# Kernel optimization log

Measured on AMD Instinct MI355X. Metric: run time of the kernel, lower is better.

The kernel has to match this reference:

```python
import jax, jax.numpy as jnp
import numpy as np

D_MODEL = 1024
H = 16
D_K = D_MODEL // H
EPS = 1e-8


def _feature_map(x):
    # elu(x) + 1 (Performer/linear-attention positive feature map)
    return jax.nn.elu(x) + 1.0


def setup_inputs() -> dict:
    key = jax.random.key(0)
    ks = jax.random.split(key, 8)
    B, L = 4, 2048
    q = jax.random.normal(ks[0], (B, L, D_MODEL), dtype=jnp.float32)
    k = jax.random.normal(ks[1], (B, L, D_MODEL), dtype=jnp.float32)
    v = jax.random.normal(ks[2], (B, L, D_MODEL), dtype=jnp.float32)
    mask = jnp.ones((B, 1, 1, L), dtype=bool)
    s = 1.0 / np.sqrt(D_MODEL)
    w_q = jax.random.normal(ks[3], (D_MODEL, D_MODEL), dtype=jnp.float32) * s
    w_k = jax.random.normal(ks[4], (D_MODEL, D_MODEL), dtype=jnp.float32) * s
    w_v = jax.random.normal(ks[5], (D_MODEL, D_MODEL), dtype=jnp.float32) * s
    w_o = jax.random.normal(ks[6], (D_MODEL, D_MODEL), dtype=jnp.float32) * s
    return {"q": q, "k": k, "v": v, "mask": mask,
            "w_q": w_q, "w_k": w_k, "w_v": w_v, "w_o": w_o}


def reference(q, k, v, mask, w_q, w_k, w_v, w_o):
    # Linear (use_Linear=True) branch of MultiHeadAttentionBlock.forward.
    B, Lq, _ = q.shape
    Lk = k.shape[1]
    # fused-style projections (torch Linear: x @ W.T), split into heads -> bhnd
    query = (q @ w_q.T).reshape(B, Lq, H, D_K).transpose(0, 2, 1, 3)
    key_  = (k @ w_k.T).reshape(B, Lk, H, D_K).transpose(0, 2, 1, 3)
    value = (v @ w_v.T).reshape(B, Lk, H, D_K).transpose(0, 2, 1, 3)

    Q = _feature_map(query)            # [B,H,Lq,d_k]
    K = _feature_map(key_)             # [B,H,Lk,d_k]
    KV = jnp.einsum('bhnd,bhnm->bhdm', K, value)           # [B,H,d_k,d_k]
    Z = 1.0 / (jnp.einsum('bhnd,bhd->bhn', Q, K.sum(axis=2)) + EPS)  # [B,H,Lq]
    out = jnp.einsum('bhnd,bhdm,bhn->bhnm', Q, KV, Z)      # [B,H,Lq,d_k]

    out = out.transpose(0, 2, 1, 3).reshape(B, Lq, D_MODEL)
    return out @ w_o.T
```

## Files before the change

### kernel.cpp

```cpp
#include <hip/hip_runtime.h>
#include <cstdint>
#include <cstddef>

typedef __bf16 bf16;
typedef __bf16 bf16x8 __attribute__((ext_vector_type(8)));
typedef __bf16 bf16x4 __attribute__((ext_vector_type(4)));
typedef float  f32x4  __attribute__((ext_vector_type(4)));

#define DM     1024
#define MROWS  8192
#define LSEQ   2048
#define NBATCH 4
#define NHEAD  16
#define BHEADS 64
#define KV_S   8
#define KVT_STRIDE 4160

__device__ __forceinline__ void async16(const void* g, void* l) {
    __builtin_amdgcn_global_load_lds(
        (const __attribute__((address_space(1))) void*)g,
        (__attribute__((address_space(3))) void*)l, 16, 0, 0);
}

struct CastArgs {
    const float* s[7];
    bf16*        d[7];
    int          nblk[7];
};

__global__ __launch_bounds__(256) void cast_all(CastArgs a) {
    const int z = blockIdx.z;
    if ((int)blockIdx.x >= a.nblk[z]) return;
    const int i = blockIdx.x * 256 + threadIdx.x;
    float4 f = ((const float4*)a.s[z])[i];
    bf16x4 o; o[0] = (bf16)f.x; o[1] = (bf16)f.y; o[2] = (bf16)f.z; o[3] = (bf16)f.w;
    ((bf16x4*)a.d[z])[i] = o;
}

struct GemmArgs {
    const bf16* A[3];
    const bf16* B[3];
    void*       C[3];
    int         mode[3];
    int         Ndim;
    int         Kdim;
};

__global__ __launch_bounds__(256) void gemm_nt(GemmArgs args) {
    const int z = blockIdx.z;
    const bf16* __restrict__ A  = args.A[z];
    const bf16* __restrict__ Bm = args.B[z];
    void* Cp = args.C[z];
    const int mode = args.mode[z];
    const int N = args.Ndim, K = args.Kdim;

    __shared__ __attribute__((aligned(16))) bf16 sA[128 * 64];
    __shared__ __attribute__((aligned(16))) bf16 sB[128 * 64];

    const int tid  = threadIdx.x;
    const int wave = tid >> 6;
    const int lane = tid & 63;
    const int wm = wave >> 1, wn = wave & 1;

    const int fb = blockIdx.x + 8 * (int)blockIdx.y;
    const int bx = (fb >> 3) & 7;
    const int by = (fb & 7) * 8 + (fb >> 6);
    const int row0 = by * 128;
    const int col0 = bx * 128;

    const int rr = lane >> 3;
    const int cc = lane & 7;
    const int csw = ((cc ^ rr) * 8);
    const bf16* gA = A  + (size_t)(row0 + wave * 32 + rr) * K + csw;
    const bf16* gB = Bm + (size_t)(col0 + wave * 32 + rr) * K + csw;

    f32x4 acc[4][4] = {};

    const int lr = lane & 15;
    const int qd = lane >> 4;
    const int swz = lr & 7;

    for (int k0 = 0; k0 < K; k0 += 64) {
        #pragma unroll
        for (int j = 0; j < 4; ++j) {
            async16(gA + k0 + (size_t)(j * 8) * K, &sA[(wave * 32 + j * 8) * 64]);
            async16(gB + k0 + (size_t)(j * 8) * K, &sB[(wave * 32 + j * 8) * 64]);
        }
        __syncthreads();

        #pragma unroll
        for (int ks = 0; ks < 2; ++ks) {
            bf16x8 af[4], bfr[4];
            #pragma unroll
            for (int mi = 0; mi < 4; ++mi)
                af[mi] = *(const bf16x8*)&sA[(wm * 64 + mi * 16 + lr) * 64 + (((ks * 4 + qd) ^ swz) * 8)];
            #pragma unroll
            for (int ni = 0; ni < 4; ++ni)
                bfr[ni] = *(const bf16x8*)&sB[(wn * 64 + ni * 16 + lr) * 64 + (((ks * 4 + qd) ^ swz) * 8)];
            #pragma unroll
            for (int mi = 0; mi < 4; ++mi)
                #pragma unroll
                for (int ni = 0; ni < 4; ++ni)
                    acc[mi][ni] = __builtin_amdgcn_mfma_f32_16x16x32_bf16(af[mi], bfr[ni], acc[mi][ni], 0, 0, 0);
        }
        __syncthreads();
    }

    #pragma unroll
    for (int mi = 0; mi < 4; ++mi) {
        #pragma unroll
        for (int ni = 0; ni < 4; ++ni) {
            #pragma unroll
            for (int r = 0; r < 4; ++r) {
                const int grow = row0 + wm * 64 + mi * 16 + qd * 4 + r;
                const int gcol = col0 + wn * 64 + ni * 16 + lr;
                float val = acc[mi][ni][r];
                if (mode == 1) val = (val > 0.f) ? (val + 1.f) : __expf(val);
                if (mode == 2) ((float*)Cp)[(size_t)grow * N + gcol] = val;
                else           ((bf16*)Cp)[(size_t)grow * N + gcol] = (bf16)val;
            }
        }
    }
}

__global__ __launch_bounds__(256) void kv_partial(const bf16* __restrict__ Kp,
                                                  const bf16* __restrict__ Vp,
                                                  float* __restrict__ KVTp) {
    const int bh = blockIdx.x, s = blockIdx.y;
    const int b = bh >> 4, h = bh & 15;
    const int tid = threadIdx.x;
    const int m  = tid & 63;
    const int dg = tid >> 6;

    __shared__ float sK[32][64];
    __shared__ float sV[32][64];

    float acc[16] = {};
    float ks = 0.f;

    const int rr = tid >> 3;
    const int cc = (tid & 7) * 8;

    const size_t rowbase = (size_t)(b * LSEQ + s * 256) * DM + h * 64;

    for (int c = 0; c < 8; ++c) {
        {
            const size_t g = rowbase + (size_t)(c * 32 + rr) * DM + cc;
            bf16x8 k8 = *(const bf16x8*)&Kp[g];
            bf16x8 v8 = *(const bf16x8*)&Vp[g];
            float4 kf0 = {(float)k8[0], (float)k8[1], (float)k8[2], (float)k8[3]};
            float4 kf1 = {(float)k8[4], (float)k8[5], (float)k8[6], (float)k8[7]};
            float4 vf0 = {(float)v8[0], (float)v8[1], (float)v8[2], (float)v8[3]};
            float4 vf1 = {(float)v8[4], (float)v8[5], (float)v8[6], (float)v8[7]};
            *(float4*)&sK[rr][cc]     = kf0;
            *(float4*)&sK[rr][cc + 4] = kf1;
            *(float4*)&sV[rr][cc]     = vf0;
            *(float4*)&sV[rr][cc + 4] = vf1;
        }
        __syncthreads();
        #pragma unroll 4
        for (int n = 0; n < 32; ++n) {
            const float vv = sV[n][m];
            const float4* pk = (const float4*)&sK[n][dg * 16];
            #pragma unroll
            for (int t4 = 0; t4 < 4; ++t4) {
                float4 kk = pk[t4];
                acc[t4 * 4 + 0] += vv * kk.x;
                acc[t4 * 4 + 1] += vv * kk.y;
                acc[t4 * 4 + 2] += vv * kk.z;
                acc[t4 * 4 + 3] += vv * kk.w;
            }
            if (dg == 0) ks += sK[n][m];
        }
        __syncthreads();
    }

    float* outp = &KVTp[(size_t)(bh * KV_S + s) * KVT_STRIDE];
    #pragma unroll
    for (int t4 = 0; t4 < 4; ++t4) {
        float4 o = {acc[t4 * 4 + 0], acc[t4 * 4 + 1], acc[t4 * 4 + 2], acc[t4 * 4 + 3]};
        *(float4*)&outp[m * 64 + dg * 16 + t4 * 4] = o;
    }
    if (dg == 0) outp[4096 + m] = ks;
}

__global__ __launch_bounds__(256) void kv_reduce(const float* __restrict__ KVTp,
                                                 bf16* __restrict__ KVT,
                                                 float* __restrict__ Ksum) {
    const int bh = blockIdx.x;
    const int idx = blockIdx.y * 256 + threadIdx.x;
    if (idx >= KVT_STRIDE) return;
    float s = 0.f;
    #pragma unroll
    for (int p = 0; p < KV_S; ++p) s += KVTp[(size_t)(bh * KV_S + p) * KVT_STRIDE + idx];
    if (idx < 4096) KVT[(size_t)bh * 4096 + idx] = (bf16)s;
    else            Ksum[bh * 64 + (idx - 4096)] = s;
}

__global__ __launch_bounds__(256) void attn_out(const bf16* __restrict__ Qp,
                                                const bf16* __restrict__ KVT,
                                                const float* __restrict__ Ksum,
                                                bf16* __restrict__ Ab) {
    const int bh = blockIdx.y;
    const int b = bh >> 4, h = bh & 15;
    const int row0 = blockIdx.x * 128;
    const int tid = threadIdx.x, wave = tid >> 6, lane = tid & 63;

    __shared__ __attribute__((aligned(16))) bf16 sQ[128 * 64];
    __shared__ __attribute__((aligned(16))) bf16 sKV[64 * 64];
    __shared__ float sKs[64];

    const int rr8 = lane >> 3;
    const int cc8 = lane & 7;
    const int csw = ((cc8 ^ rr8) * 8);

    const bf16* qbase = &Qp[(size_t)(b * LSEQ + row0) * DM + h * 64];
    #pragma unroll
    for (int j = 0; j < 4; ++j) {
        const int r0 = wave * 32 + j * 8;
        async16(qbase + (size_t)(r0 + rr8) * DM + csw, &sQ[r0 * 64]);
    }
    const bf16* kvbase = &KVT[(size_t)bh * 4096];
    #pragma unroll
    for (int j = 0; j < 2; ++j) {
        const int r0 = wave * 16 + j * 8;
        async16(kvbase + (r0 + rr8) * 64 + csw, &sKV[r0 * 64]);
    }
    if (tid < 64) sKs[tid] = Ksum[bh * 64 + tid];
    __syncthreads();

    const int zrow = lane >> 1;
    const int dh = lane & 1;
    float zacc = 0.f;
    {
        const bf16* qr = &sQ[(wave * 32 + zrow) * 64];
        #pragma unroll
        for (int c = 0; c < 4; ++c) {
            const int chunk = dh * 4 + c;
            bf16x8 q8 = *(const bf16x8*)&qr[(chunk ^ (zrow & 7)) * 8];
            const float* ksp = &sKs[chunk * 8];
            #pragma unroll
            for (int j = 0; j < 8; ++j) zacc += (float)q8[j] * ksp[j];
        }
    }
    zacc += __shfl_xor(zacc, 1, 64);
    const float zinv = 1.0f / (zacc + 1e-8f);

    f32x4 acc[2][4] = {};
    const int lr = lane & 15, qd = lane >> 4;
    const int swz = lr & 7;
    #pragma unroll
    for (int ks = 0; ks < 2; ++ks) {
        bf16x8 af[2], bfr[4];
        #pragma unroll
        for (int mi = 0; mi < 2; ++mi)
            af[mi] = *(const bf16x8*)&sQ[(wave * 32 + mi * 16 + lr) * 64 + (((ks * 4 + qd) ^ swz) * 8)];
        #pragma unroll
        for (int ni = 0; ni < 4; ++ni)
            bfr[ni] = *(const bf16x8*)&sKV[(ni * 16 + lr) * 64 + (((ks * 4 + qd) ^ swz) * 8)];
        #pragma unroll
        for (int mi = 0; mi < 2; ++mi)
            #pragma unroll
            for (int ni = 0; ni < 4; ++ni)
                acc[mi][ni] = __builtin_amdgcn_mfma_f32_16x16x32_bf16(af[mi], bfr[ni], acc[mi][ni], 0, 0, 0);
    }

    #pragma unroll
    for (int mi = 0; mi < 2; ++mi) {
        #pragma unroll
        for (int rr = 0; rr < 4; ++rr) {
            const int rlocal = mi * 16 + qd * 4 + rr;
            const float zv = __shfl(zinv, rlocal * 2, 64);
            const int nrow = row0 + wave * 32 + rlocal;
            #pragma unroll
            for (int ni = 0; ni < 4; ++ni)
                Ab[(size_t)(b * LSEQ + nrow) * DM + h * 64 + ni * 16 + lr] =
                    (bf16)(acc[mi][ni][rr] * zv);
        }
    }
}

extern "C" void kernel_launch(void* const* d_in, const int* in_sizes, int n_in,
                              void* d_out, int out_size, void* d_ws, size_t ws_size,
                              hipStream_t stream) {
    const float* q  = (const float*)d_in[0];
    const float* k  = (const float*)d_in[1];
    const float* v  = (const float*)d_in[2];
    const float* wq = (const float*)d_in[4];
    const float* wk = (const float*)d_in[5];
    const float* wv = (const float*)d_in[6];
    const float* wo = (const float*)d_in[7];

    char* ws = (char*)d_ws;
    size_t off = 0;
    auto alloc = [&](size_t bytes) -> void* {
        void* p = ws + off;
        off += (bytes + 255) & ~(size_t)255;
        return p;
    };

    bf16* qb   = (bf16*)alloc((size_t)MROWS * DM * 2);
    bf16* kb   = (bf16*)alloc((size_t)MROWS * DM * 2);
    bf16* vb   = (bf16*)alloc((size_t)MROWS * DM * 2);
    bf16* wqb  = (bf16*)alloc((size_t)DM * DM * 2);
    bf16* wkb  = (bf16*)alloc((size_t)DM * DM * 2);
    bf16* wvb  = (bf16*)alloc((size_t)DM * DM * 2);
    bf16* wob  = (bf16*)alloc((size_t)DM * DM * 2);
    bf16* Qp   = (bf16*)alloc((size_t)MROWS * DM * 2);
    bf16* Kp   = (bf16*)alloc((size_t)MROWS * DM * 2);
    bf16* Vp   = (bf16*)alloc((size_t)MROWS * DM * 2);
    bf16* Ab   = (bf16*)alloc((size_t)MROWS * DM * 2);
    float* KVTp = (float*)alloc((size_t)BHEADS * KV_S * KVT_STRIDE * 4);
    bf16* KVT  = (bf16*)alloc((size_t)BHEADS * 4096 * 2);
    float* Ksum = (float*)alloc((size_t)BHEADS * 64 * 4);

    CastArgs ca;
    ca.s[0] = q;  ca.s[1] = k;  ca.s[2] = v;  ca.s[3] = wq; ca.s[4] = wk; ca.s[5] = wv; ca.s[6] = wo;
    ca.d[0] = qb; ca.d[1] = kb; ca.d[2] = vb; ca.d[3] = wqb; ca.d[4] = wkb; ca.d[5] = wvb; ca.d[6] = wob;
    const int nb_big = MROWS * DM / 4 / 256, nb_w = DM * DM / 4 / 256;
    ca.nblk[0] = nb_big; ca.nblk[1] = nb_big; ca.nblk[2] = nb_big;
    ca.nblk[3] = nb_w; ca.nblk[4] = nb_w; ca.nblk[5] = nb_w; ca.nblk[6] = nb_w;
    cast_all<<<dim3(nb_big, 1, 7), 256, 0, stream>>>(ca);

    GemmArgs pa;
    pa.A[0] = qb;  pa.A[1] = kb;  pa.A[2] = vb;
    pa.B[0] = wqb; pa.B[1] = wkb; pa.B[2] = wvb;
    pa.C[0] = Qp;  pa.C[1] = Kp;  pa.C[2] = Vp;
    pa.mode[0] = 1; pa.mode[1] = 1; pa.mode[2] = 0;
    pa.Ndim = DM; pa.Kdim = DM;
    gemm_nt<<<dim3(DM / 128, MROWS / 128, 3), 256, 0, stream>>>(pa);

    kv_partial<<<dim3(BHEADS, KV_S), 256, 0, stream>>>(Kp, Vp, KVTp);
    kv_reduce<<<dim3(BHEADS, (KVT_STRIDE + 255) / 256), 256, 0, stream>>>(KVTp, KVT, Ksum);

    attn_out<<<dim3(LSEQ / 128, BHEADS), 256, 0, stream>>>(Qp, KVT, Ksum, Ab);

    GemmArgs fa;
    fa.A[0] = Ab; fa.A[1] = nullptr; fa.A[2] = nullptr;
    fa.B[0] = wob; fa.B[1] = nullptr; fa.B[2] = nullptr;
    fa.C[0] = d_out; fa.C[1] = nullptr; fa.C[2] = nullptr;
    fa.mode[0] = 2; fa.mode[1] = 0; fa.mode[2] = 0;
    fa.Ndim = DM; fa.Kdim = DM;
    gemm_nt<<<dim3(DM / 128, MROWS / 128, 1), 256, 0, stream>>>(fa);
}
```

Measured before the change: 299.6 us.

## Write K/V projections head-transposed and compute KV with MFMA; add narrow final GEMM

The K and V projection GEMM epilogue now writes per-head transposed layouts ([b,h,d,n]), so the KV outer-product reduction can load contiguous tiles asynchronously into LDS and use bf16 MFMA instead of scalar fp32 FMAs. The final output projection gets its own kernel with 128x64 tiles, doubling the block count to improve CU occupancy, and it writes fp32 directly. The GEMM also drops runtime N/K parameters in favour of constants. The risks are strided 8-byte scattered stores in the transposed epilogue and bf16 inputs to the KV product instead of fp32 accumulation of bf16 values, though accumulation stays fp32.

```diff
diff --git a/kernel.cpp b/kernel.cpp
--- a/kernel.cpp
+++ b/kernel.cpp
@@ -42,8 +42,6 @@
     const bf16* B[3];
     void*       C[3];
     int         mode[3];
-    int         Ndim;
-    int         Kdim;
 };
 
 __global__ __launch_bounds__(256) void gemm_nt(GemmArgs args) {
@@ -52,7 +50,7 @@
     const bf16* __restrict__ Bm = args.B[z];
     void* Cp = args.C[z];
     const int mode = args.mode[z];
-    const int N = args.Ndim, K = args.Kdim;
+    const int K = DM;
 
     __shared__ __attribute__((aligned(16))) bf16 sA[128 * 64];
     __shared__ __attribute__((aligned(16))) bf16 sB[128 * 64];
@@ -106,82 +104,170 @@
         __syncthreads();
     }
 
-    #pragma unroll
-    for (int mi = 0; mi < 4; ++mi) {
-        #pragma unroll
-        for (int ni = 0; ni < 4; ++ni) {
+    if (mode >= 3) {
+        #pragma unroll
+        for (int mi = 0; mi < 4; ++mi) {
+            const int grow0 = row0 + wm * 64 + mi * 16 + qd * 4;
+            const int b  = grow0 >> 11;
+            const int n0 = grow0 & 2047;
+            #pragma unroll
+            for (int ni = 0; ni < 4; ++ni) {
+                const int gcol = col0 + wn * 64 + ni * 16 + lr;
+                const int h = gcol >> 6;
+                const int d = gcol & 63;
+                bf16x4 o;
+                #pragma unroll
+                for (int r = 0; r < 4; ++r) {
+                    float val = acc[mi][ni][r];
+                    if (mode == 4) val = (val > 0.f) ? (val + 1.f) : __expf(val);
+                    o[r] = (bf16)val;
+                }
+                *(bf16x4*)&((bf16*)Cp)[(size_t)((b * 16 + h) * 64 + d) * 2048 + n0] = o;
+            }
+        }
+    } else {
+        #pragma unroll
+        for (int mi = 0; mi < 4; ++mi) {
+            #pragma unroll
+            for (int ni = 0; ni < 4; ++ni) {
+                #pragma unroll
+                for (int r = 0; r < 4; ++r) {
+                    const int grow = row0 + wm * 64 + mi * 16 + qd * 4 + r;
+                    const int gcol = col0 + wn * 64 + ni * 16 + lr;
+                    float val = acc[mi][ni][r];
+                    if (mode == 1) val = (val > 0.f) ? (val + 1.f) : __expf(val);
+                    ((bf16*)Cp)[(size_t)grow * DM + gcol] = (bf16)val;
+                }
+            }
+        }
+    }
+}
+
+__global__ __launch_bounds__(256) void gemm_fin(const bf16* __restrict__ A,
+                                                const bf16* __restrict__ Bm,
+                                                float* __restrict__ C) {
+    const int K = DM;
+    __shared__ __attribute__((aligned(16))) bf16 sA[128 * 64];
+    __shared__ __attribute__((aligned(16))) bf16 sB[64 * 64];
+
+    const int tid  = threadIdx.x;
+    const int wave = tid >> 6;
+    const int lane = tid & 63;
+    const int wm = wave >> 1, wn = wave & 1;
+
+    const int fb = blockIdx.x + 16 * (int)blockIdx.y;
+    const int xcd = fb & 7;
+    const int g = fb >> 3;
+    const int bx = g & 15;
+    const int by = xcd * 8 + (g >> 4);
+    const int row0 = by * 128;
+    const int col0 = bx * 64;
+
+    const int rr = lane >> 3;
+    const int cc = lane & 7;
+    const int csw = ((cc ^ rr) * 8);
+    const bf16* gA = A  + (size_t)(row0 + wave * 32 + rr) * K + csw;
+    const bf16* gB = Bm + (size_t)(col0 + wave * 16 + rr) * K + csw;
+
+    f32x4 acc[4][2] = {};
+
+    const int lr = lane & 15;
+    const int qd = lane >> 4;
+    const int swz = lr & 7;
+
+    for (int k0 = 0; k0 < K; k0 += 64) {
+        #pragma unroll
+        for (int j = 0; j < 4; ++j)
+            async16(gA + k0 + (size_t)(j * 8) * K, &sA[(wave * 32 + j * 8) * 64]);
+        #pragma unroll
+        for (int j = 0; j < 2; ++j)
+            async16(gB + k0 + (size_t)(j * 8) * K, &sB[(wave * 16 + j * 8) * 64]);
+        __syncthreads();
+
+        #pragma unroll
+        for (int ks = 0; ks < 2; ++ks) {
+            bf16x8 af[4], bfr[2];
+            #pragma unroll
+            for (int mi = 0; mi < 4; ++mi)
+                af[mi] = *(const bf16x8*)&sA[(wm * 64 + mi * 16 + lr) * 64 + (((ks * 4 + qd) ^ swz) * 8)];
+            #pragma unroll
+            for (int ni = 0; ni < 2; ++ni)
+                bfr[ni] = *(const bf16x8*)&sB[(wn * 32 + ni * 16 + lr) * 64 + (((ks * 4 + qd) ^ swz) * 8)];
+            #pragma unroll
+            for (int mi = 0; mi < 4; ++mi)
+                #pragma unroll
+                for (int ni = 0; ni < 2; ++ni)
+                    acc[mi][ni] = __builtin_amdgcn_mfma_f32_16x16x32_bf16(af[mi], bfr[ni], acc[mi][ni], 0, 0, 0);
+        }
+        __syncthreads();
+    }
+
+    #pragma unroll
+    for (int mi = 0; mi < 4; ++mi)
+        #pragma unroll
+        for (int ni = 0; ni < 2; ++ni)
             #pragma unroll
             for (int r = 0; r < 4; ++r) {
                 const int grow = row0 + wm * 64 + mi * 16 + qd * 4 + r;
-                const int gcol = col0 + wn * 64 + ni * 16 + lr;
-                float val = acc[mi][ni][r];
-                if (mode == 1) val = (val > 0.f) ? (val + 1.f) : __expf(val);
-                if (mode == 2) ((float*)Cp)[(size_t)grow * N + gcol] = val;
-                else           ((bf16*)Cp)[(size_t)grow * N + gcol] = (bf16)val;
+                const int gcol = col0 + wn * 32 + ni * 16 + lr;
+                C[(size_t)grow * DM + gcol] = acc[mi][ni][r];
             }
-        }
-    }
-}
-
-__global__ __launch_bounds__(256) void kv_partial(const bf16* __restrict__ Kp,
-                                                  const bf16* __restrict__ Vp,
-                                                  float* __restrict__ KVTp) {
+}
+
+__global__ __launch_bounds__(256) void kv_mfma(const bf16* __restrict__ KpT,
+                                               const bf16* __restrict__ VpT,
+                                               float* __restrict__ KVTp) {
     const int bh = blockIdx.x, s = blockIdx.y;
-    const int b = bh >> 4, h = bh & 15;
-    const int tid = threadIdx.x;
-    const int m  = tid & 63;
-    const int dg = tid >> 6;
-
-    __shared__ float sK[32][64];
-    __shared__ float sV[32][64];
-
-    float acc[16] = {};
-    float ks = 0.f;
-
-    const int rr = tid >> 3;
-    const int cc = (tid & 7) * 8;
-
-    const size_t rowbase = (size_t)(b * LSEQ + s * 256) * DM + h * 64;
-
-    for (int c = 0; c < 8; ++c) {
-        {
-            const size_t g = rowbase + (size_t)(c * 32 + rr) * DM + cc;
-            bf16x8 k8 = *(const bf16x8*)&Kp[g];
-            bf16x8 v8 = *(const bf16x8*)&Vp[g];
-            float4 kf0 = {(float)k8[0], (float)k8[1], (float)k8[2], (float)k8[3]};
-            float4 kf1 = {(float)k8[4], (float)k8[5], (float)k8[6], (float)k8[7]};
-            float4 vf0 = {(float)v8[0], (float)v8[1], (float)v8[2], (float)v8[3]};
-            float4 vf1 = {(float)v8[4], (float)v8[5], (float)v8[6], (float)v8[7]};
-            *(float4*)&sK[rr][cc]     = kf0;
-            *(float4*)&sK[rr][cc + 4] = kf1;
-            *(float4*)&sV[rr][cc]     = vf0;
-            *(float4*)&sV[rr][cc + 4] = vf1;
-        }
-        __syncthreads();
-        #pragma unroll 4
-        for (int n = 0; n < 32; ++n) {
-            const float vv = sV[n][m];
-            const float4* pk = (const float4*)&sK[n][dg * 16];
-            #pragma unroll
-            for (int t4 = 0; t4 < 4; ++t4) {
-                float4 kk = pk[t4];
-                acc[t4 * 4 + 0] += vv * kk.x;
-                acc[t4 * 4 + 1] += vv * kk.y;
-                acc[t4 * 4 + 2] += vv * kk.z;
-                acc[t4 * 4 + 3] += vv * kk.w;
-            }
-            if (dg == 0) ks += sK[n][m];
-        }
-        __syncthreads();
+    const int tid = threadIdx.x, wave = tid >> 6, lane = tid & 63;
+
+    __shared__ __attribute__((aligned(16))) bf16 sVT[64 * 256];
+    __shared__ __attribute__((aligned(16))) bf16 sKT[64 * 256];
+
+    const int dd = lane >> 5;
+    const int c  = lane & 31;
+    #pragma unroll
+    for (int j = 0; j < 8; ++j) {
+        const int i2 = (wave * 8 + j) * 2;
+        const int r  = i2 + dd;
+        const int cs = (c ^ (r & 7)) * 8;
+        const size_t gofs = (size_t)(bh * 64 + r) * 2048 + s * 256 + cs;
+        async16(VpT + gofs, &sVT[i2 * 256]);
+        async16(KpT + gofs, &sKT[i2 * 256]);
+    }
+    __syncthreads();
+
+    const int lr = lane & 15, qd = lane >> 4;
+    f32x4 acc[4] = {};
+    const int rA = wave * 16 + lr;
+    #pragma unroll
+    for (int k0 = 0; k0 < 8; ++k0) {
+        const int ch = k0 * 4 + qd;
+        bf16x8 a = *(const bf16x8*)&sVT[rA * 256 + ((ch ^ (rA & 7)) * 8)];
+        #pragma unroll
+        for (int ni = 0; ni < 4; ++ni) {
+            const int rB = ni * 16 + lr;
+            bf16x8 b = *(const bf16x8*)&sKT[rB * 256 + ((ch ^ (rB & 7)) * 8)];
+            acc[ni] = __builtin_amdgcn_mfma_f32_16x16x32_bf16(a, b, acc[ni], 0, 0, 0);
+        }
     }
 
     float* outp = &KVTp[(size_t)(bh * KV_S + s) * KVT_STRIDE];
     #pragma unroll
-    for (int t4 = 0; t4 < 4; ++t4) {
-        float4 o = {acc[t4 * 4 + 0], acc[t4 * 4 + 1], acc[t4 * 4 + 2], acc[t4 * 4 + 3]};
-        *(float4*)&outp[m * 64 + dg * 16 + t4 * 4] = o;
-    }
-    if (dg == 0) outp[4096 + m] = ks;
+    for (int ni = 0; ni < 4; ++ni)
+        #pragma unroll
+        for (int r = 0; r < 4; ++r)
+            outp[(wave * 16 + qd * 4 + r) * 64 + ni * 16 + lr] = acc[ni][r];
+
+    if (wave == 0) {
+        float ks = 0.f;
+        #pragma unroll
+        for (int c2 = 0; c2 < 32; ++c2) {
+            bf16x8 kk = *(const bf16x8*)&sKT[lane * 256 + ((c2 ^ (lane & 7)) * 8)];
+            #pragma unroll
+            for (int j = 0; j < 8; ++j) ks += (float)kk[j];
+        }
+        outp[4096 + lane] = ks;
+    }
 }
 
 __global__ __launch_bounds__(256) void kv_reduce(const float* __restrict__ KVTp,
@@ -307,8 +393,8 @@
     bf16* wvb  = (bf16*)alloc((size_t)DM * DM * 2);
     bf16* wob  = (bf16*)alloc((size_t)DM * DM * 2);
     bf16* Qp   = (bf16*)alloc((size_t)MROWS * DM * 2);
-    bf16* Kp   = (bf16*)alloc((size_t)MROWS * DM * 2);
-    bf16* Vp   = (bf16*)alloc((size_t)MROWS * DM * 2);
+    bf16* KpT  = (bf16*)alloc((size_t)MROWS * DM * 2);
+    bf16* VpT  = (bf16*)alloc((size_t)MROWS * DM * 2);
     bf16* Ab   = (bf16*)alloc((size_t)MROWS * DM * 2);
     float* KVTp = (float*)alloc((size_t)BHEADS * KV_S * KVT_STRIDE * 4);
     bf16* KVT  = (bf16*)alloc((size_t)BHEADS * 4096 * 2);
@@ -325,21 +411,14 @@
     GemmArgs pa;
     pa.A[0] = qb;  pa.A[1] = kb;  pa.A[2] = vb;
     pa.B[0] = wqb; pa.B[1] = wkb; pa.B[2] = wvb;
-    pa.C[0] = Qp;  pa.C[1] = Kp;  pa.C[2] = Vp;
-    pa.mode[0] = 1; pa.mode[1] = 1; pa.mode[2] = 0;
-    pa.Ndim = DM; pa.Kdim = DM;
+    pa.C[0] = Qp;  pa.C[1] = KpT; pa.C[2] = VpT;
+    pa.mode[0] = 1; pa.mode[1] = 4; pa.mode[2] = 3;
     gemm_nt<<<dim3(DM / 128, MROWS / 128, 3), 256, 0, stream>>>(pa);
 
-    kv_partial<<<dim3(BHEADS, KV_S), 256, 0, stream>>>(Kp, Vp, KVTp);
+    kv_mfma<<<dim3(BHEADS, KV_S), 256, 0, stream>>>(KpT, VpT, KVTp);
     kv_reduce<<<dim3(BHEADS, (KVT_STRIDE + 255) / 256), 256, 0, stream>>>(KVTp, KVT, Ksum);
 
     attn_out<<<dim3(LSEQ / 128, BHEADS), 256, 0, stream>>>(Qp, KVT, Ksum, Ab);
 
-    GemmArgs fa;
-    fa.A[0] = Ab; fa.A[1] = nullptr; fa.A[2] = nullptr;
-    fa.B[0] = wob; fa.B[1] = nullptr; fa.B[2] = nullptr;
-    fa.C[0] = d_out; fa.C[1] = nullptr; fa.C[2] = nullptr;
-    fa.mode[0] = 2; fa.mode[1] = 0; fa.mode[2] = 0;
-    fa.Ndim = DM; fa.Kdim = DM;
-    gemm_nt<<<dim3(DM / 128, MROWS / 128, 1), 256, 0, stream>>>(fa);
-}
+    gemm_fin<<<dim3(DM / 64, MROWS / 128), 256, 0, stream>>>(Ab, wob, (float*)d_out);
+}
```

Result: faster. 264.7 us (-11.7%).
